# Kernel optimization log

Measured on AMD Instinct MI355X. Metric: run time of the kernel, lower is better.

Reference implementation:

```python
import jax, jax.numpy as jnp
import numpy as np

NUM_JOINTS = 33
EPS = 1e-5
# MediaPipe 33-landmark pose skeleton connections
SKELETON_EDGES = np.array([
    [0,1],[1,2],[2,3],[3,7],[0,4],[4,5],[5,6],[6,8],[9,10],
    [11,12],[11,13],[13,15],[15,17],[15,19],[15,21],[17,19],
    [12,14],[14,16],[16,18],[16,20],[16,22],[18,20],
    [11,23],[12,24],[23,24],[23,25],[24,26],[25,27],[26,28],
    [27,29],[28,30],[29,31],[30,32],[27,31],[28,32]], dtype=np.int64)


def _batched_edges(B):
    und = np.concatenate([SKELETON_EDGES, SKELETON_EDGES[:, ::-1]], axis=0)
    loops = np.stack([np.arange(NUM_JOINTS)] * 2, axis=1)
    e = np.concatenate([und, loops], axis=0)  # [103, 2] per graph (incl. self loops)
    eb = (e[None, :, :] + (np.arange(B) * NUM_JOINTS)[:, None, None]).reshape(-1, 2)
    return jnp.asarray(eb[:, 0], dtype=jnp.int32), jnp.asarray(eb[:, 1], dtype=jnp.int32)


def setup_inputs() -> dict:
    key = jax.random.key(0)
    B, N, F, H, L = 4096, NUM_JOINTS, 256, 256, 4
    ks = jax.random.split(key, 20)
    d = {"x": jax.random.normal(ks[0], (B, N, F), dtype=jnp.float32)}
    dims = [(F, H), (H, H), (H, H)]
    i = 1
    for li, (di, do) in enumerate(dims):
        d[f"w{li}"] = jax.random.normal(ks[i], (di, do), dtype=jnp.float32) * 0.05; i += 1
        d[f"b{li}"] = jnp.zeros((do,), dtype=jnp.float32)
        d[f"g{li}"] = jnp.ones((do,), dtype=jnp.float32)
        d[f"be{li}"] = jnp.zeros((do,), dtype=jnp.float32)
    d["wh"] = jax.random.normal(ks[i], (H, H), dtype=jnp.float32) * 0.05; i += 1
    d["bh"] = jnp.zeros((H,), dtype=jnp.float32)
    d["wc"] = jax.random.normal(ks[i], (H, L), dtype=jnp.float32) * 0.05; i += 1
    d["bc"] = jnp.zeros((L,), dtype=jnp.float32)
    src, dst = _batched_edges(B)
    d["src"], d["dst"] = src, dst
    return d


def _gcn_conv(x, W, b, src, dst, norm, num_nodes):
    h = x @ W                          # [NN, out]
    msg = h[src] * norm[:, None]       # gather + scale
    agg = jax.ops.segment_sum(msg, dst, num_segments=num_nodes)
    return agg + b


def _bn_relu(x, g, be):
    mu = jnp.mean(x, axis=0)
    var = jnp.mean((x - mu) ** 2, axis=0)  # biased, torch training BN
    return jax.nn.relu((x - mu) * jax.lax.rsqrt(var + EPS) * g + be)


def reference(x, w0, b0, g0, be0, w1, b1, g1, be1, w2, b2, g2, be2, wh, bh, wc, bc, src, dst):
    B, N, F = x.shape
    NN = B * N
    h = jnp.nan_to_num(x.reshape(NN, F))
    # symmetric GCN normalization D^{-1/2}(A+I)D^{-1/2}; self loops already in edge list
    deg = jax.ops.segment_sum(jnp.ones_like(src, dtype=h.dtype), dst, num_segments=NN)
    dinv = jax.lax.rsqrt(deg)
    norm = dinv[src] * dinv[dst]
    for W, b, g, be in ((w0, b0, g0, be0), (w1, b1, g1, be1), (w2, b2, g2, be2)):
        h = _gcn_conv(h, W, b, src, dst, norm, NN)
        h = _bn_relu(h, g, be)  # dropout: eval mode -> identity
    h = _gcn_conv(h, wh, bh, src, dst, norm, NN)
    pooled = h.reshape(B, N, -1).mean(axis=1)  # global mean pool per graph
    return pooled @ wc + bc
```

## Files before the change

kernel.cpp:

```cpp
#include <hip/hip_runtime.h>

typedef unsigned short u16;
typedef __attribute__((ext_vector_type(8))) short short8;
typedef __attribute__((ext_vector_type(4))) float floatx4;

#define NN_TOT 135168

static constexpr int NBCNT[33] = {2,2,2,2,2,2,2,1,1,1,1,3,3,2,2,4,4,2,2,2,2,1,1,3,3,2,2,3,3,2,2,2,2};
static constexpr int NBR[33][4] = {
 {1,4,0,0},{0,2,0,0},{1,3,0,0},{2,7,0,0},{0,5,0,0},{4,6,0,0},{5,8,0,0},
 {3,0,0,0},{6,0,0,0},{10,0,0,0},{9,0,0,0},
 {12,13,23,0},{11,14,24,0},{11,15,0,0},{12,16,0,0},
 {13,17,19,21},{14,18,20,22},
 {15,19,0,0},{16,20,0,0},{15,17,0,0},{16,18,0,0},{15,0,0,0},{16,0,0,0},
 {11,24,25,0},{12,23,26,0},{23,27,0,0},{24,28,0,0},
 {25,29,31,0},{26,30,32,0},{27,31,0,0},{28,32,0,0},{29,27,0,0},{30,28,0,0}};
static constexpr float R2 = 0.70710678f, R3 = 0.57735027f, R4 = 0.5f, R5 = 0.44721360f;
static constexpr float DINV[33] = {R3,R3,R3,R3,R3,R3,R3, R2,R2,R2,R2, R4,R4, R3,R3, R5,R5,
                                   R3,R3,R3,R3, R2,R2, R4,R4, R3,R3, R4,R4, R3,R3,R3,R3};

__device__ __forceinline__ float bf2f(u16 u) {
  unsigned int v = ((unsigned int)u) << 16; float f; __builtin_memcpy(&f, &v, 4); return f;
}
__device__ __forceinline__ u16 f2bf(float f) {
  unsigned int u; __builtin_memcpy(&u, &f, 4);
  return (u16)((u + 0x7fffu + ((u >> 16) & 1u)) >> 16);
}
__device__ __forceinline__ float ldin(const void* p, int i, int isbf) {
  return isbf ? bf2f(((const u16*)p)[i]) : ((const float*)p)[i];
}
__device__ __forceinline__ void gload_lds16(const u16* g, u16* l) {
  __builtin_amdgcn_global_load_lds((const __attribute__((address_space(1))) unsigned int*)g,
                                   (__attribute__((address_space(3))) unsigned int*)l, 16, 0, 0);
}

__global__ __launch_bounds__(256) void detect_kernel(const u16* __restrict__ x,
                                                     int* __restrict__ flag)
{
  __shared__ int cnt[256];
  const int t = threadIdx.x;
  int c = 0;
  for (int j = 0; j < 16; ++j) {
    u16 u = x[(t*16 + j)*2];
    int e = (u >> 7) & 0xFF;
    c += (e >= 118 && e <= 130) ? 1 : 0;
  }
  cnt[t] = c;
  __syncthreads();
  if (t == 0) {
    int s = 0;
    for (int i = 0; i < 256; ++i) s += cnt[i];
    *flag = (s > 2048) ? 1 : 0;
  }
}

__global__ __launch_bounds__(256) void transpose_kernel(const void* __restrict__ w0,
    const void* __restrict__ w1, const void* __restrict__ w2, u16* __restrict__ Wt,
    const int* __restrict__ flag)
{
  const int m = blockIdx.x >> 4;
  const int nb = (blockIdx.x & 15) * 16;
  const void* W = m == 0 ? w0 : (m == 1 ? w1 : w2);
  u16* O = Wt + (size_t)m * 65536;
  const int t = threadIdx.x;
  const int lane = t & 63, wv = t >> 6;
  const int isbf = *flag;
  if (isbf) {
    const u16* Wb = (const u16*)W;
#pragma unroll
    for (int nn = 0; nn < 4; ++nn) {
      const int n = nb + nn*4 + wv;
#pragma unroll
      for (int j = 0; j < 4; ++j) {
        const int k = lane + 64*j;
        O[n*256 + k] = Wb[k*256 + n];
      }
    }
  } else {
    const float* Wf = (const float*)W;
#pragma unroll
    for (int nn = 0; nn < 4; ++nn) {
      const int n = nb + nn*4 + wv;
#pragma unroll
      for (int j = 0; j < 4; ++j) {
        const int k = lane + 64*j;
        O[n*256 + k] = f2bf(Wf[k*256 + n]);
      }
    }
  }
}

__global__ __launch_bounds__(256) void init_kernel(const void* __restrict__ wh,
    const void* __restrict__ bh, const void* __restrict__ wc, const void* __restrict__ bc,
    float* __restrict__ wq, float* __restrict__ bq, float* __restrict__ repl,
    const int* __restrict__ flag)
{
  const int idx = blockIdx.x*256 + threadIdx.x;
  for (int i = idx; i < 3*64*512; i += 65*256) repl[i] = 0.f;
  const int isbf = *flag;
  const int t = threadIdx.x;
  const int lane = t & 63;
  if (blockIdx.x < 64) {
    const int r = blockIdx.x*4 + (t >> 6);
    float a0=0.f, a1=0.f, a2=0.f, a3=0.f;
#pragma unroll
    for (int j = 0; j < 4; ++j) {
      const int k = lane + 64*j;
      const float w = ldin(wh, r*256 + k, isbf);
      a0 += w*ldin(wc, k*4+0, isbf); a1 += w*ldin(wc, k*4+1, isbf);
      a2 += w*ldin(wc, k*4+2, isbf); a3 += w*ldin(wc, k*4+3, isbf);
    }
#pragma unroll
    for (int off = 32; off; off >>= 1) {
      a0 += __shfl_xor(a0, off); a1 += __shfl_xor(a1, off);
      a2 += __shfl_xor(a2, off); a3 += __shfl_xor(a3, off);
    }
    if (lane == 0) { wq[r*4+0]=a0; wq[r*4+1]=a1; wq[r*4+2]=a2; wq[r*4+3]=a3; }
  } else if (t < 64) {
    float s0=0.f, s1=0.f, s2=0.f, s3=0.f;
#pragma unroll
    for (int j = 0; j < 4; ++j) {
      const int k = lane + 64*j;
      const float b = ldin(bh, k, isbf);
      s0 += b*ldin(wc, k*4+0, isbf); s1 += b*ldin(wc, k*4+1, isbf);
      s2 += b*ldin(wc, k*4+2, isbf); s3 += b*ldin(wc, k*4+3, isbf);
    }
#pragma unroll
    for (int off = 32; off; off >>= 1) {
      s0 += __shfl_xor(s0, off); s1 += __shfl_xor(s1, off);
      s2 += __shfl_xor(s2, off); s3 += __shfl_xor(s3, off);
    }
    if (lane == 0) {
      bq[0] = s0 + ldin(bc, 0, isbf); bq[1] = s1 + ldin(bc, 1, isbf);
      bq[2] = s2 + ldin(bc, 2, isbf); bq[3] = s3 + ldin(bc, 3, isbf);
    }
  }
}

template<int ACT>
__global__ __launch_bounds__(256, 2) void gemm_kernel(
    const void* __restrict__ Ag, const u16* __restrict__ Bt,
    const float* __restrict__ fscale, const float* __restrict__ fshift,
    u16* __restrict__ T, const int* __restrict__ flag)
{
  __shared__ __align__(16) u16 sA[128*32];
  __shared__ __align__(16) u16 sB[256*32];
  const int tid = threadIdx.x;
  const int lane = tid & 63, wid = tid >> 6;
  const int wm = wid >> 1, wn = wid & 1;
  const size_t m0 = (size_t)blockIdx.x * 128;
  const int isbf = (ACT == 0) ? *flag : 1;

  floatx4 acc[4][8];
#pragma unroll
  for (int i = 0; i < 4; ++i)
#pragma unroll
    for (int j = 0; j < 8; ++j) acc[i][j] = (floatx4){0.f, 0.f, 0.f, 0.f};

  const int r0 = tid >> 2;
  const int c8 = (tid & 3) * 8;
  const int lr = lane >> 2;
  const int lc = (lane & 3) * 8;
  const int fr = lane & 15, q = lane >> 4;

  for (int kc = 0; kc < 8; ++kc) {
    const int k0 = kc * 32;
    __syncthreads();
    if (ACT == 0) {
      if (isbf) {
        const u16* Ab = (const u16*)Ag;
#pragma unroll
        for (int i = 0; i < 2; ++i)
          gload_lds16(Ab + (m0 + wid*32 + i*16 + lr)*256 + k0 + lc,
                      sA + (wid*32 + i*16)*32);
      } else {
        const float* Af = (const float*)Ag;
#pragma unroll
        for (int rr = 0; rr < 2; ++rr) {
          const int r = r0 + rr*64;
          float4 p0 = *(const float4*)(Af + (m0 + r)*256 + k0 + c8);
          float4 p1 = *(const float4*)(Af + (m0 + r)*256 + k0 + c8 + 4);
          u16 ov[8];
          ov[0]=f2bf(p0.x); ov[1]=f2bf(p0.y); ov[2]=f2bf(p0.z); ov[3]=f2bf(p0.w);
          ov[4]=f2bf(p1.x); ov[5]=f2bf(p1.y); ov[6]=f2bf(p1.z); ov[7]=f2bf(p1.w);
          *(uint4*)(sA + r*32 + c8) = *(const uint4*)ov;
        }
      }
    } else {
      const u16* Ab = (const u16*)Ag;
      float scv[8], shv[8];
#pragma unroll
      for (int j = 0; j < 8; ++j) { scv[j] = fscale[k0 + c8 + j]; shv[j] = fshift[k0 + c8 + j]; }
#pragma unroll
      for (int rr = 0; rr < 2; ++rr) {
        const int r = r0 + rr*64;
        uint4 pk = *(const uint4*)(Ab + (m0 + r)*256 + k0 + c8);
        const u16* us = (const u16*)&pk;
        u16 ov[8];
#pragma unroll
        for (int j = 0; j < 8; ++j) {
          float f = bf2f(us[j]);
          f = fmaxf(0.f, fmaf(f, scv[j], shv[j]));
          ov[j] = f2bf(f);
        }
        *(uint4*)(sA + r*32 + c8) = *(const uint4*)ov;
      }
    }
#pragma unroll
    for (int i = 0; i < 4; ++i)
      gload_lds16(Bt + (wid*64 + i*16 + lr)*256 + k0 + lc,
                  sB + (wid*64 + i*16)*32);
    __syncthreads();

    short8 a[4], b[8];
#pragma unroll
    for (int mf = 0; mf < 4; ++mf) a[mf] = *(const short8*)(sA + (wm*64 + mf*16 + fr)*32 + q*8);
#pragma unroll
    for (int nf = 0; nf < 8; ++nf) b[nf] = *(const short8*)(sB + (wn*128 + nf*16 + fr)*32 + q*8);
#pragma unroll
    for (int mf = 0; mf < 4; ++mf)
#pragma unroll
      for (int nf = 0; nf < 8; ++nf)
        acc[mf][nf] = __builtin_amdgcn_mfma_f32_16x16x32_bf16(a[mf], b[nf], acc[mf][nf], 0, 0, 0);
  }

#pragma unroll
  for (int mf = 0; mf < 4; ++mf)
#pragma unroll
    for (int nf = 0; nf < 8; ++nf)
#pragma unroll
      for (int r = 0; r < 4; ++r) {
        const size_t row = m0 + wm*64 + mf*16 + q*4 + r;
        const int col = wn*128 + nf*16 + fr;
        T[row*256 + col] = f2bf(acc[mf][nf][r]);
      }
}

__global__ __launch_bounds__(256) void agg_kernel(const u16* __restrict__ T,
    const void* __restrict__ bias, u16* __restrict__ H, float* __restrict__ repl,
    const int* __restrict__ flag)
{
  const int g = blockIdx.x, c = threadIdx.x;
  const int isbf = *flag;
  const u16* tg = T + (size_t)g * (33*256);
  u16* hg = H + (size_t)g * (33*256);
  float acc[33];
#pragma unroll
  for (int d = 0; d < 33; ++d) acc[d] = 0.f;
#pragma unroll
  for (int s = 0; s < 33; ++s) {
    float v = bf2f(tg[s*256 + c]) * DINV[s];
    acc[s] += v;
#pragma unroll
    for (int i = 0; i < NBCNT[s]; ++i) acc[NBR[s][i]] += v;
  }
  const float bv = ldin(bias, c, isbf);
  float s1 = 0.f, s2 = 0.f;
#pragma unroll
  for (int d = 0; d < 33; ++d) {
    float o = fmaf(acc[d], DINV[d], bv);
    hg[d*256 + c] = f2bf(o);
    s1 += o; s2 += o*o;
  }
  float* r1 = repl + (size_t)(g & 63) * 512;
  atomicAdd(r1 + c, s1);
  atomicAdd(r1 + 256 + c, s2);
}

__global__ __launch_bounds__(256) void statfin_kernel(const float* __restrict__ repl,
    const void* __restrict__ gamma, const void* __restrict__ beta, float* __restrict__ fs,
    const int* __restrict__ flag)
{
  const int c = threadIdx.x;
  const int isbf = *flag;
  float s1 = 0.f, s2 = 0.f;
  for (int r = 0; r < 64; ++r) { s1 += repl[r*512 + c]; s2 += repl[r*512 + 256 + c]; }
  const float inv = 1.f / (float)NN_TOT;
  const float mu = s1 * inv;
  const float var = s2 * inv - mu*mu;
  const float rs = rsqrtf(var + 1e-5f);
  const float sc = rs * ldin(gamma, c, isbf);
  fs[c] = sc;
  fs[256 + c] = ldin(beta, c, isbf) - mu * sc;
}

__global__ __launch_bounds__(256) void final_kernel(const u16* __restrict__ H,
    const float* __restrict__ fs, const float* __restrict__ wq,
    const float* __restrict__ bq, void* __restrict__ outp,
    const int* __restrict__ flag)
{
  const int g = blockIdx.x, c = threadIdx.x;
  const int isbf = *flag;
  const float sc = fs[c], sh = fs[256 + c];
  const u16* hg = H + (size_t)g * (33*256);
  float v = 0.f;
#pragma unroll
  for (int s = 0; s < 33; ++s) {
    float a = DINV[s];
#pragma unroll
    for (int i = 0; i < NBCNT[s]; ++i) a += DINV[NBR[s][i]];
    const float w = DINV[s] * a * (1.f/33.f);
    float x = bf2f(hg[s*256 + c]);
    x = fmaxf(0.f, fmaf(x, sc, sh));
    v += w * x;
  }
  float p0 = v*wq[c*4+0], p1 = v*wq[c*4+1], p2 = v*wq[c*4+2], p3 = v*wq[c*4+3];
#pragma unroll
  for (int off = 32; off; off >>= 1) {
    p0 += __shfl_xor(p0, off);
    p1 += __shfl_xor(p1, off);
    p2 += __shfl_xor(p2, off);
    p3 += __shfl_xor(p3, off);
  }
  __shared__ float sred[4][4];
  const int lane = c & 63, wid = c >> 6;
  if (lane == 0) { sred[wid][0]=p0; sred[wid][1]=p1; sred[wid][2]=p2; sred[wid][3]=p3; }
  __syncthreads();
  if (c < 4) {
    float r = sred[0][c] + sred[1][c] + sred[2][c] + sred[3][c] + bq[c];
    if (isbf) ((u16*)outp)[(size_t)g*4 + c] = f2bf(r);
    else      ((float*)outp)[(size_t)g*4 + c] = r;
  }
}

extern "C" void kernel_launch(void* const* d_in, const int* in_sizes, int n_in,
                              void* d_out, int out_size, void* d_ws, size_t ws_size,
                              hipStream_t stream)
{
  const void* x   = d_in[0];
  const void* w0  = d_in[1];
  const void* b0  = d_in[2];
  const void* g0  = d_in[3];
  const void* be0 = d_in[4];
  const void* w1  = d_in[5];
  const void* b1  = d_in[6];
  const void* g1  = d_in[7];
  const void* be1 = d_in[8];
  const void* w2  = d_in[9];
  const void* b2  = d_in[10];
  const void* g2  = d_in[11];
  const void* be2 = d_in[12];
  const void* wh  = d_in[13];
  const void* bh  = d_in[14];
  const void* wc  = d_in[15];
  const void* bc  = d_in[16];

  char* ws = (char*)d_ws;
  float* wq   = (float*)(ws + 0);
  float* bq   = (float*)(ws + 4096);
  float* fs   = (float*)(ws + 4608);
  int*   flag = (int*)  (ws + 12288);
  float* repl = (float*)(ws + 16384);
  u16*   Wt   = (u16*)  (ws + 409600);
  u16*   A    = (u16*)  (ws + 802816);
  (void)in_sizes; (void)n_in; (void)out_size; (void)ws_size;

  detect_kernel<<<1, 256, 0, stream>>>((const u16*)x, flag);
  transpose_kernel<<<48, 256, 0, stream>>>(w0, w1, w2, Wt, flag);
  init_kernel<<<65, 256, 0, stream>>>(wh, bh, wc, bc, wq, bq, repl, flag);

  gemm_kernel<0><<<1056, 256, 0, stream>>>(x, Wt, nullptr, nullptr, A, flag);
  agg_kernel<<<4096, 256, 0, stream>>>(A, b0, A, repl, flag);
  statfin_kernel<<<1, 256, 0, stream>>>(repl, g0, be0, fs, flag);
  gemm_kernel<1><<<1056, 256, 0, stream>>>(A, Wt + 65536, fs, fs + 256, A, flag);
  agg_kernel<<<4096, 256, 0, stream>>>(A, b1, A, repl + 32768, flag);
  statfin_kernel<<<1, 256, 0, stream>>>(repl + 32768, g1, be1, fs + 512, flag);
  gemm_kernel<1><<<1056, 256, 0, stream>>>(A, Wt + 131072, fs + 512, fs + 768, A, flag);
  agg_kernel<<<4096, 256, 0, stream>>>(A, b2, A, repl + 65536, flag);
  statfin_kernel<<<1, 256, 0, stream>>>(repl + 65536, g2, be2, fs + 1024, flag);
  final_kernel<<<4096, 256, 0, stream>>>(A, fs + 1024, wq, bq, d_out, flag);
}
```

Before: 459.9 us.

## Fuse GCN aggregation into GEMM by aggregating inputs before the matmul

Reorders each GCN layer as (Â·X)·W instead of Â·(X·W). Each block handles two 33-node graphs (66 rows, padded to 80) and builds the normalized neighbor sum while staging A into LDS. Bias add and batch-norm statistics move into the GEMM epilogue, so the separate agg_kernel and its extra write and read of the intermediate activation are removed. In exchange, each row is re-read up to five times per k-chunk (mostly expected to hit in cache), the padding wastes MFMA work, and the per-warp tile shrinks to 64 columns.

```diff
diff --git a/kernel.cpp b/kernel.cpp
--- a/kernel.cpp
+++ b/kernel.cpp
@@ -138,133 +138,147 @@
 }
 
 template<int ACT>
-__global__ __launch_bounds__(256, 2) void gemm_kernel(
-    const void* __restrict__ Ag, const u16* __restrict__ Bt,
+__global__ __launch_bounds__(256, 2) void gcn_kernel(
+    const void* __restrict__ Ain, const u16* __restrict__ Bt,
     const float* __restrict__ fscale, const float* __restrict__ fshift,
-    u16* __restrict__ T, const int* __restrict__ flag)
-{
-  __shared__ __align__(16) u16 sA[128*32];
+    const void* __restrict__ bias, u16* __restrict__ Hout,
+    float* __restrict__ repl, const int* __restrict__ flag)
+{
+  __shared__ __align__(16) u16 sA[80*32];
   __shared__ __align__(16) u16 sB[256*32];
   const int tid = threadIdx.x;
   const int lane = tid & 63, wid = tid >> 6;
-  const int wm = wid >> 1, wn = wid & 1;
-  const size_t m0 = (size_t)blockIdx.x * 128;
+  const int fr = lane & 15, q = lane >> 4;
+  const int n0 = wid * 64;
   const int isbf = (ACT == 0) ? *flag : 1;
-
-  floatx4 acc[4][8];
-#pragma unroll
-  for (int i = 0; i < 4; ++i)
-#pragma unroll
-    for (int j = 0; j < 8; ++j) acc[i][j] = (floatx4){0.f, 0.f, 0.f, 0.f};
-
-  const int r0 = tid >> 2;
-  const int c8 = (tid & 3) * 8;
-  const int lr = lane >> 2;
-  const int lc = (lane & 3) * 8;
-  const int fr = lane & 15, q = lane >> 4;
+  const size_t row0 = (size_t)blockIdx.x * 66;
+
+  if (tid < 56) *(uint4*)(sA + 66*32 + tid*8) = (uint4){0,0,0,0};
+
+  const int sr = tid >> 1;
+  const int sc0 = (tid & 1) * 16;
+  const bool stg = (sr < 66);
+  int srcs[5]; float wts[5];
+  {
+    const int rmc = (sr < 33) ? sr : ((sr < 66) ? sr - 33 : 0);
+    const int rbase = (sr < 33) ? 0 : 33;
+    const float di = DINV[rmc];
+    srcs[0] = rbase + rmc; wts[0] = di * di;
+#pragma unroll
+    for (int j = 0; j < 4; ++j) {
+      if (j < NBCNT[rmc]) { const int s = NBR[rmc][j]; srcs[j+1] = rbase + s; wts[j+1] = di * DINV[s]; }
+      else { srcs[j+1] = rbase; wts[j+1] = 0.f; }
+    }
+  }
+
+  floatx4 acc[5][4];
+#pragma unroll
+  for (int mt = 0; mt < 5; ++mt)
+#pragma unroll
+    for (int nt = 0; nt < 4; ++nt) acc[mt][nt] = (floatx4){0.f,0.f,0.f,0.f};
 
   for (int kc = 0; kc < 8; ++kc) {
     const int k0 = kc * 32;
     __syncthreads();
-    if (ACT == 0) {
+#pragma unroll
+    for (int i = 0; i < 4; ++i)
+      gload_lds16(Bt + (wid*64 + i*16 + (lane>>2))*256 + k0 + (lane&3)*8,
+                  sB + (wid*64 + i*16)*32);
+    if (stg) {
+      float av[16];
+#pragma unroll
+      for (int e = 0; e < 16; ++e) av[e] = 0.f;
+      float scv[16], shv[16];
+      if (ACT == 1) {
+#pragma unroll
+        for (int e = 0; e < 16; ++e) { scv[e] = fscale[k0 + sc0 + e]; shv[e] = fshift[k0 + sc0 + e]; }
+      }
       if (isbf) {
-        const u16* Ab = (const u16*)Ag;
-#pragma unroll
-        for (int i = 0; i < 2; ++i)
-          gload_lds16(Ab + (m0 + wid*32 + i*16 + lr)*256 + k0 + lc,
-                      sA + (wid*32 + i*16)*32);
+        const u16* Ab = (const u16*)Ain;
+#pragma unroll
+        for (int j = 0; j < 5; ++j) {
+          const u16* sp = Ab + (row0 + srcs[j])*256 + k0 + sc0;
+          uint4 p0 = *(const uint4*)sp;
+          uint4 p1 = *(const uint4*)(sp + 8);
+          const u16* u0 = (const u16*)&p0;
+          const u16* u1 = (const u16*)&p1;
+          const float w = wts[j];
+#pragma unroll
+          for (int e = 0; e < 8; ++e) {
+            float f0 = bf2f(u0[e]), f1 = bf2f(u1[e]);
+            if (ACT == 1) {
+              f0 = fmaxf(0.f, fmaf(f0, scv[e], shv[e]));
+              f1 = fmaxf(0.f, fmaf(f1, scv[e+8], shv[e+8]));
+            }
+            av[e] += w * f0; av[e+8] += w * f1;
+          }
+        }
       } else {
-        const float* Af = (const float*)Ag;
-#pragma unroll
-        for (int rr = 0; rr < 2; ++rr) {
-          const int r = r0 + rr*64;
-          float4 p0 = *(const float4*)(Af + (m0 + r)*256 + k0 + c8);
-          float4 p1 = *(const float4*)(Af + (m0 + r)*256 + k0 + c8 + 4);
-          u16 ov[8];
-          ov[0]=f2bf(p0.x); ov[1]=f2bf(p0.y); ov[2]=f2bf(p0.z); ov[3]=f2bf(p0.w);
-          ov[4]=f2bf(p1.x); ov[5]=f2bf(p1.y); ov[6]=f2bf(p1.z); ov[7]=f2bf(p1.w);
-          *(uint4*)(sA + r*32 + c8) = *(const uint4*)ov;
+        const float* Af = (const float*)Ain;
+#pragma unroll
+        for (int j = 0; j < 5; ++j) {
+          const float* sp = Af + (row0 + srcs[j])*256 + k0 + sc0;
+          const float w = wts[j];
+#pragma unroll
+          for (int v = 0; v < 4; ++v) {
+            float4 p = *(const float4*)(sp + v*4);
+            av[v*4+0] += w * p.x; av[v*4+1] += w * p.y;
+            av[v*4+2] += w * p.z; av[v*4+3] += w * p.w;
+          }
         }
       }
-    } else {
-      const u16* Ab = (const u16*)Ag;
-      float scv[8], shv[8];
-#pragma unroll
-      for (int j = 0; j < 8; ++j) { scv[j] = fscale[k0 + c8 + j]; shv[j] = fshift[k0 + c8 + j]; }
-#pragma unroll
-      for (int rr = 0; rr < 2; ++rr) {
-        const int r = r0 + rr*64;
-        uint4 pk = *(const uint4*)(Ab + (m0 + r)*256 + k0 + c8);
-        const u16* us = (const u16*)&pk;
-        u16 ov[8];
-#pragma unroll
-        for (int j = 0; j < 8; ++j) {
-          float f = bf2f(us[j]);
-          f = fmaxf(0.f, fmaf(f, scv[j], shv[j]));
-          ov[j] = f2bf(f);
+      u16 ov[16];
+#pragma unroll
+      for (int e = 0; e < 16; ++e) ov[e] = f2bf(av[e]);
+      *(uint4*)(sA + sr*32 + sc0)     = *(const uint4*)(ov);
+      *(uint4*)(sA + sr*32 + sc0 + 8) = *(const uint4*)(ov + 8);
+    }
+    __syncthreads();
+
+    short8 a[5], b[4];
+#pragma unroll
+    for (int mt = 0; mt < 5; ++mt) a[mt] = *(const short8*)(sA + (mt*16 + fr)*32 + q*8);
+#pragma unroll
+    for (int nt = 0; nt < 4; ++nt) b[nt] = *(const short8*)(sB + (n0 + nt*16 + fr)*32 + q*8);
+#pragma unroll
+    for (int mt = 0; mt < 5; ++mt)
+#pragma unroll
+      for (int nt = 0; nt < 4; ++nt)
+        acc[mt][nt] = __builtin_amdgcn_mfma_f32_16x16x32_bf16(a[mt], b[nt], acc[mt][nt], 0, 0, 0);
+  }
+
+  float bv[4], s1[4], s2[4];
+#pragma unroll
+  for (int nt = 0; nt < 4; ++nt) {
+    bv[nt] = ldin(bias, n0 + nt*16 + fr, *flag);
+    s1[nt] = 0.f; s2[nt] = 0.f;
+  }
+#pragma unroll
+  for (int mt = 0; mt < 5; ++mt)
+#pragma unroll
+    for (int nt = 0; nt < 4; ++nt)
+#pragma unroll
+      for (int rr = 0; rr < 4; ++rr) {
+        const int row = mt*16 + q*4 + rr;
+        if (row < 66) {
+          const float h = acc[mt][nt][rr] + bv[nt];
+          Hout[(row0 + row)*256 + n0 + nt*16 + fr] = f2bf(h);
+          s1[nt] += h; s2[nt] += h*h;
         }
-        *(uint4*)(sA + r*32 + c8) = *(const uint4*)ov;
-      }
-    }
-#pragma unroll
-    for (int i = 0; i < 4; ++i)
-      gload_lds16(Bt + (wid*64 + i*16 + lr)*256 + k0 + lc,
-                  sB + (wid*64 + i*16)*32);
-    __syncthreads();
-
-    short8 a[4], b[8];
-#pragma unroll
-    for (int mf = 0; mf < 4; ++mf) a[mf] = *(const short8*)(sA + (wm*64 + mf*16 + fr)*32 + q*8);
-#pragma unroll
-    for (int nf = 0; nf < 8; ++nf) b[nf] = *(const short8*)(sB + (wn*128 + nf*16 + fr)*32 + q*8);
-#pragma unroll
-    for (int mf = 0; mf < 4; ++mf)
-#pragma unroll
-      for (int nf = 0; nf < 8; ++nf)
-        acc[mf][nf] = __builtin_amdgcn_mfma_f32_16x16x32_bf16(a[mf], b[nf], acc[mf][nf], 0, 0, 0);
-  }
-
-#pragma unroll
-  for (int mf = 0; mf < 4; ++mf)
-#pragma unroll
-    for (int nf = 0; nf < 8; ++nf)
-#pragma unroll
-      for (int r = 0; r < 4; ++r) {
-        const size_t row = m0 + wm*64 + mf*16 + q*4 + r;
-        const int col = wn*128 + nf*16 + fr;
-        T[row*256 + col] = f2bf(acc[mf][nf][r]);
-      }
-}
-
-__global__ __launch_bounds__(256) void agg_kernel(const u16* __restrict__ T,
-    const void* __restrict__ bias, u16* __restrict__ H, float* __restrict__ repl,
-    const int* __restrict__ flag)
-{
-  const int g = blockIdx.x, c = threadIdx.x;
-  const int isbf = *flag;
-  const u16* tg = T + (size_t)g * (33*256);
-  u16* hg = H + (size_t)g * (33*256);
-  float acc[33];
-#pragma unroll
-  for (int d = 0; d < 33; ++d) acc[d] = 0.f;
-#pragma unroll
-  for (int s = 0; s < 33; ++s) {
-    float v = bf2f(tg[s*256 + c]) * DINV[s];
-    acc[s] += v;
-#pragma unroll
-    for (int i = 0; i < NBCNT[s]; ++i) acc[NBR[s][i]] += v;
-  }
-  const float bv = ldin(bias, c, isbf);
-  float s1 = 0.f, s2 = 0.f;
-#pragma unroll
-  for (int d = 0; d < 33; ++d) {
-    float o = fmaf(acc[d], DINV[d], bv);
-    hg[d*256 + c] = f2bf(o);
-    s1 += o; s2 += o*o;
-  }
-  float* r1 = repl + (size_t)(g & 63) * 512;
-  atomicAdd(r1 + c, s1);
-  atomicAdd(r1 + 256 + c, s2);
+      }
+#pragma unroll
+  for (int nt = 0; nt < 4; ++nt) {
+    s1[nt] += __shfl_xor(s1[nt], 16); s1[nt] += __shfl_xor(s1[nt], 32);
+    s2[nt] += __shfl_xor(s2[nt], 16); s2[nt] += __shfl_xor(s2[nt], 32);
+  }
+  if (lane < 16) {
+    float* r1 = repl + (size_t)(blockIdx.x & 63) * 512;
+#pragma unroll
+    for (int nt = 0; nt < 4; ++nt) {
+      atomicAdd(r1 + n0 + nt*16 + fr, s1[nt]);
+      atomicAdd(r1 + 256 + n0 + nt*16 + fr, s2[nt]);
+    }
+  }
 }
 
 __global__ __launch_bounds__(256) void statfin_kernel(const float* __restrict__ repl,
@@ -359,14 +373,11 @@
   transpose_kernel<<<48, 256, 0, stream>>>(w0, w1, w2, Wt, flag);
   init_kernel<<<65, 256, 0, stream>>>(wh, bh, wc, bc, wq, bq, repl, flag);
 
-  gemm_kernel<0><<<1056, 256, 0, stream>>>(x, Wt, nullptr, nullptr, A, flag);
-  agg_kernel<<<4096, 256, 0, stream>>>(A, b0, A, repl, flag);
+  gcn_kernel<0><<<2048, 256, 0, stream>>>(x, Wt, nullptr, nullptr, b0, A, repl, flag);
   statfin_kernel<<<1, 256, 0, stream>>>(repl, g0, be0, fs, flag);
-  gemm_kernel<1><<<1056, 256, 0, stream>>>(A, Wt + 65536, fs, fs + 256, A, flag);
-  agg_kernel<<<4096, 256, 0, stream>>>(A, b1, A, repl + 32768, flag);
+  gcn_kernel<1><<<2048, 256, 0, stream>>>(A, Wt + 65536, fs, fs + 256, b1, A, repl + 32768, flag);
   statfin_kernel<<<1, 256, 0, stream>>>(repl + 32768, g1, be1, fs + 512, flag);
-  gemm_kernel<1><<<1056, 256, 0, stream>>>(A, Wt + 131072, fs + 512, fs + 768, A, flag);
-  agg_kernel<<<4096, 256, 0, stream>>>(A, b2, A, repl + 65536, flag);
+  gcn_kernel<1><<<2048, 256, 0, stream>>>(A, Wt + 131072, fs + 512, fs + 768, b2, A, repl + 65536, flag);
   statfin_kernel<<<1, 256, 0, stream>>>(repl + 65536, g2, be2, fs + 1024, flag);
   final_kernel<<<4096, 256, 0, stream>>>(A, fs + 1024, wq, bq, d_out, flag);
 }
```

After: 501.0 us. 8.9% more time.
